# Performance work log

Hardware: AMD Instinct MI355X
Metric: run time of the kernel (lower is better)

## Reference

```python
import jax, jax.numpy as jnp
import numpy as np

B, N, E = 32, 2048, 1048576  # 32 uniform graphs of 2048 nodes, avg degree 16
BN = B * N
KS = (1024, 512, 256)  # TopKPooling ratio=0.5 -> ceil(0.5*n) per layer (uniform graphs -> static)


def _mlp2(x, w1, b1, w2, b2):
    # nn.Sequential(Linear, ReLU, Linear)
    return jnp.maximum(x @ w1 + b1, 0.0) @ w2 + b2


def _forward(x, edge_attr, node_w1, node_b1, node_w2, node_b2,
             edge_w1, edge_b1, edge_w2, edge_b2,
             eff_in_w, eff_in_b, eff_h_w, eff_h_b, eff_out_w, eff_out_b,
             upd_in_w, upd_in_b, upd_h_w, upd_h_b, upd_out_w, upd_out_b,
             pool_w, edge_index):
    relu = lambda t: jnp.maximum(t, 0.0)
    src, dst = edge_index[0], edge_index[1]  # PyG: x_j = h[src], x_i = h[dst], aggregate at dst
    h = _mlp2(x, node_w1, node_b1, node_w2, node_b2)          # [BN, F] node embedding
    e = _mlp2(edge_attr, edge_w1, edge_b1, edge_w2, edge_b2)  # [E, F]  edge embedding
    node_mask = jnp.ones((BN,), bool)
    edge_mask = jnp.ones((E,), bool)
    for i in range(3):
        # --- DPIGNNLayer: gather-concat-MLP(+edge_attr) message, scatter-mean aggregate ---
        m = jnp.concatenate([h[dst], h[src]], axis=-1)        # [E, 2F] = cat(x_i, x_j)
        m = relu(m @ eff_in_w[i] + eff_in_b[i])
        m = relu(m @ eff_h_w[i] + eff_h_b[i])
        m = relu(m @ eff_out_w[i] + eff_out_b[i] + e)
        em = edge_mask.astype(h.dtype)[:, None]
        agg = jax.ops.segment_sum(m * em, dst, num_segments=BN)
        cnt = jax.ops.segment_sum(em, dst, num_segments=BN)
        mean = agg / jnp.maximum(cnt, 1.0)                    # mean aggr (0 where no edges)
        u = jnp.concatenate([mean, h], axis=-1)
        u = relu(u @ upd_in_w[i] + upd_in_b[i])
        u = relu(u @ upd_h_w[i] + upd_h_b[i])
        _ = relu(u @ upd_out_w[i] + upd_out_b[i] + h)  # dead compute: source update() returns x
        # --- TopKPooling(ratio=0.5), masked form (uniform graph sizes -> static k) ---
        w = pool_w[i]
        score = jnp.tanh((h @ w) / jnp.linalg.norm(w))        # [BN]
        masked = jnp.where(node_mask, score, -jnp.inf).reshape(B, N)
        _, idx = jax.lax.top_k(masked, KS[i])                 # [B, k]
        sel = jnp.zeros((B, N), bool).at[jnp.arange(B)[:, None], idx].set(True).reshape(-1)
        node_mask = sel
        h = jnp.where(node_mask[:, None], h * score[:, None], 0.0)
        edge_mask = edge_mask & node_mask[src] & node_mask[dst]  # filter_adj equivalent
    # global_mean_pool over surviving nodes per graph
    nm = node_mask.astype(h.dtype)[:, None]
    sums = (h * nm).reshape(B, N, -1).sum(axis=1)
    cnts = nm.reshape(B, N, 1).sum(axis=1)
    return sums / jnp.maximum(cnts, 1.0)  # [B, F]


def setup_inputs() -> dict:
    key = jax.random.key(0)
    ks = iter(jax.random.split(key, 40))
    F, ND, ED = 128, 16, 8
    s = 0.05
    W = lambda shape: jax.random.normal(next(ks), shape, jnp.float32) * s
    zb = lambda shape: jnp.zeros(shape, jnp.float32)
    e_per = E // B
    base = (jnp.arange(E) // e_per) * N  # graph offset per edge
    src = jax.random.randint(next(ks), (E,), 0, N) + base
    dst = jax.random.randint(next(ks), (E,), 0, N) + base
    return {
        'x': jax.random.normal(next(ks), (BN, ND), jnp.float32),
        'edge_attr': jax.random.normal(next(ks), (E, ED), jnp.float32),
        'node_w1': W((ND, F)), 'node_b1': zb((F,)),
        'node_w2': W((F, F)), 'node_b2': zb((F,)),
        'edge_w1': W((ED, F)), 'edge_b1': zb((F,)),
        'edge_w2': W((F, F)), 'edge_b2': zb((F,)),
        'eff_in_w': W((3, 2 * F, F)), 'eff_in_b': zb((3, F)),
        'eff_h_w': W((3, F, F)), 'eff_h_b': zb((3, F)),
        'eff_out_w': W((3, F, F)), 'eff_out_b': zb((3, F)),
        'upd_in_w': W((3, 2 * F, F)), 'upd_in_b': zb((3, F)),
        'upd_h_w': W((3, F, F)), 'upd_h_b': zb((3, F)),
        'upd_out_w': W((3, F, F)), 'upd_out_b': zb((3, F)),
        'pool_w': W((3, F)),
        'edge_index': jnp.stack([src, dst]),
    }


def reference(x, edge_attr, node_w1, node_b1, node_w2, node_b2,
              edge_w1, edge_b1, edge_w2, edge_b2,
              eff_in_w, eff_in_b, eff_h_w, eff_h_b, eff_out_w, eff_out_b,
              upd_in_w, upd_in_b, upd_h_w, upd_h_b, upd_out_w, upd_out_b,
              pool_w, edge_index):
    return _forward(x, edge_attr, node_w1, node_b1, node_w2, node_b2,
                    edge_w1, edge_b1, edge_w2, edge_b2,
                    eff_in_w, eff_in_b, eff_h_w, eff_h_b, eff_out_w, eff_out_b,
                    upd_in_w, upd_in_b, upd_h_w, upd_h_b, upd_out_w, upd_out_b,
                    pool_w, edge_index)
```

## Files before the change

### kernel.cpp

```cpp
#include <hip/hip_runtime.h>
#include <hip/hip_bf16.h>


#define NPG    2048
#define NGRAPH 32
#define HPAD(b) ((b) + ((b) >> 5))

__global__ __launch_bounds__(256) void k1_fused(
    const float* __restrict__ x,
    const float* __restrict__ W1,
    const float* __restrict__ b1,
    const float* __restrict__ W2,
    const float* __restrict__ b2,
    const float* __restrict__ pw,
    float4* __restrict__ d4)
{
    __shared__ float4 sW1v[512];
    __shared__ float4 sb1v[32];
    __shared__ __align__(16) float swn[384];
    __shared__ __align__(16) float sv[384];
    __shared__ float sc[4];
    __shared__ float snorm[3];
    int t = threadIdx.x;
    int lane = t & 63, wv = t >> 6;

    for (int i = t; i < 512; i += 256) sW1v[i] = ((const float4*)W1)[i];
    if (t < 32) sb1v[t] = ((const float4*)b1)[t];
    if (wv < 3) {
        float w0 = pw[wv * 128 + lane];
        float w1 = pw[wv * 128 + 64 + lane];
        float p = w0 * w0 + w1 * w1;
        #pragma unroll
        for (int s = 32; s; s >>= 1) p += __shfl_xor(p, s);
        if (lane == 0) snorm[wv] = sqrtf(p);
    }
    __syncthreads();
    for (int i = t; i < 384; i += 256) swn[i] = pw[i] / snorm[i >> 7];
    __syncthreads();
    for (int task = t; task < 387; task += 256) {
        int k = task / 129, j = task % 129;
        const float4* r4 = (const float4*)((j < 128) ? (W2 + j * 128) : b2);
        const float* wn = swn + k * 128;
        float p0 = 0.f, p1 = 0.f, p2 = 0.f, p3 = 0.f;
        #pragma unroll 8
        for (int q = 0; q < 32; ++q) {
            float4 w = r4[q];
            p0 = fmaf(w.x, wn[4 * q + 0], p0);
            p1 = fmaf(w.y, wn[4 * q + 1], p1);
            p2 = fmaf(w.z, wn[4 * q + 2], p2);
            p3 = fmaf(w.w, wn[4 * q + 3], p3);
        }
        float p = (p0 + p1) + (p2 + p3);
        if (j < 128) sv[k * 128 + j] = p;
        else sc[k] = p;
    }
    __syncthreads();

    int n = blockIdx.x * 256 + t;
    const float4* xr = (const float4*)(x + (size_t)n * 16);
    float4 xa = xr[0], xb = xr[1], xc = xr[2], xd = xr[3];
    float xs[16] = {xa.x, xa.y, xa.z, xa.w, xb.x, xb.y, xb.z, xb.w,
                    xc.x, xc.y, xc.z, xc.w, xd.x, xd.y, xd.z, xd.w};
    const float4* sv4 = (const float4*)sv;
    float dd0 = sc[0], dd1 = sc[1], dd2 = sc[2];
    #pragma unroll 4
    for (int fq = 0; fq < 32; ++fq) {
        float4 a4 = sb1v[fq];
        #pragma unroll
        for (int j = 0; j < 16; ++j) {
            float4 w = sW1v[j * 32 + fq];
            a4.x = fmaf(xs[j], w.x, a4.x);
            a4.y = fmaf(xs[j], w.y, a4.y);
            a4.z = fmaf(xs[j], w.z, a4.z);
            a4.w = fmaf(xs[j], w.w, a4.w);
        }
        a4.x = fmaxf(a4.x, 0.f); a4.y = fmaxf(a4.y, 0.f);
        a4.z = fmaxf(a4.z, 0.f); a4.w = fmaxf(a4.w, 0.f);
        float4 v0 = sv4[fq], v1 = sv4[32 + fq], v2 = sv4[64 + fq];
        dd0 = fmaf(a4.x, v0.x, fmaf(a4.y, v0.y, fmaf(a4.z, v0.z, fmaf(a4.w, v0.w, dd0))));
        dd1 = fmaf(a4.x, v1.x, fmaf(a4.y, v1.y, fmaf(a4.z, v1.z, fmaf(a4.w, v1.w, dd1))));
        dd2 = fmaf(a4.x, v2.x, fmaf(a4.y, v2.y, fmaf(a4.z, v2.z, fmaf(a4.w, v2.w, dd2))));
    }
    d4[n] = make_float4(dd0, dd1, dd2, 0.f);
}

__global__ __launch_bounds__(1024, 1) void k2_cascade(
    const float* __restrict__ x,
    const float* __restrict__ W1,
    const float* __restrict__ b1,
    const float* __restrict__ W2,
    const float* __restrict__ b2,
    const float4* __restrict__ d4,
    float* __restrict__ out)
{
    __shared__ float d0[NPG], d1[NPG], d2[NPG];
    __shared__ float csc[NPG];
    __shared__ int alive[NPG];
    __shared__ unsigned long long key[NPG];
    __shared__ unsigned int hist[HPAD(2047) + 1];
    __shared__ int sel[256];
    __shared__ float sW1[2048];
    __shared__ float sb1[128];
    __shared__ float Spart[1024];
    __shared__ float Svec[128];
    __shared__ float red4[4];
    __shared__ unsigned long long sPrefix;
    __shared__ int sNeed;
    __shared__ int sCount;
    int t = threadIdx.x;
    int g = blockIdx.x;

    for (int n = t; n < NPG; n += 1024) {
        float4 dd = d4[g * NPG + n];
        d0[n] = dd.x; d1[n] = dd.y; d2[n] = dd.z;
        csc[n] = 1.f; alive[n] = 1;
    }
    for (int i = t; i < 2048; i += 1024) sW1[i] = W1[i];
    if (t < 128) sb1[t] = b1[t];
    if (t == 0) sCount = 0;
    __syncthreads();

    for (int r = 0; r < 3; ++r) {
        int kk = 1024 >> r;
        const float* dr = (r == 0) ? d0 : (r == 1) ? d1 : d2;
        for (int n = t; n < NPG; n += 1024) {
            unsigned long long kv = 0ull;
            if (alive[n]) {
                float z = csc[n] * dr[n];
                unsigned int bb = __float_as_uint(z);
                unsigned int m = (bb & 0x80000000u) ? ~bb : (bb | 0x80000000u);
                kv = ((unsigned long long)m << 11)
                   | (unsigned long long)(unsigned int)(2047 - n);
            }
            key[n] = kv;
        }
        if (t == 0) { sPrefix = 0ull; sNeed = kk; }
        __syncthreads();

        for (int pass = 0; pass < 4; ++pass) {
            int shift = 33 - 11 * pass;
            for (int i = t; i < HPAD(2047) + 1; i += 1024) hist[i] = 0u;
            __syncthreads();
            unsigned long long pref = sPrefix;
            unsigned int need = (unsigned int)sNeed;
            for (int n = t; n < NPG; n += 1024) {
                unsigned long long kv = key[n];
                bool cand = (pass == 0) ||
                            ((kv >> (shift + 11)) == (pref >> (shift + 11)));
                if (cand) {
                    unsigned int dgt = (unsigned int)(kv >> shift) & 2047u;
                    atomicAdd(&hist[HPAD(dgt)], 1u);
                }
            }
            __syncthreads();
            if (t < 64) {
                unsigned int h[32];
                unsigned int tl = 0;
                #pragma unroll
                for (int b = 0; b < 32; ++b) {
                    h[b] = hist[HPAD(32 * t + b)];
                    tl += h[b];
                }
                unsigned int s = tl;
                #pragma unroll
                for (int dlt = 1; dlt < 64; dlt <<= 1) {
                    unsigned int v = __shfl_down(s, dlt);
                    if (t + dlt < 64) s += v;
                }
                unsigned int above = s - tl;
                if (above < need && above + tl >= need) {
                    unsigned int cum = above;
                    #pragma unroll
                    for (int b = 31; b >= 0; --b) {
                        cum += h[b];
                        if (cum >= need) {
                            sNeed = (int)(need - (cum - h[b]));
                            sPrefix = pref |
                                ((unsigned long long)(unsigned int)(32 * t + b) << shift);
                            break;
                        }
                    }
                }
            }
            __syncthreads();
        }
        unsigned long long thr = sPrefix;
        for (int n = t; n < NPG; n += 1024) alive[n] = 0;
        __syncthreads();
        for (int n = t; n < NPG; n += 1024) {
            if (key[n] >= thr) {
                float s = tanhf(csc[n] * dr[n]);
                alive[n] = 1;
                csc[n] *= s;
                if (r == 2) sel[atomicAdd(&sCount, 1)] = n;
            }
        }
        __syncthreads();
    }

    {
        int f = t & 127, half = t >> 7;
        float Sacc = 0.f;
        for (int it = half; it < 256; it += 8) {
            int n = sel[it];
            float cn = csc[n];
            const float4* xr = (const float4*)(x + (size_t)(g * NPG + n) * 16);
            float4 xa = xr[0], xb = xr[1], xc = xr[2], xd = xr[3];
            float acc = sb1[f];
            acc = fmaf(xa.x, sW1[0 * 128 + f], acc);
            acc = fmaf(xa.y, sW1[1 * 128 + f], acc);
            acc = fmaf(xa.z, sW1[2 * 128 + f], acc);
            acc = fmaf(xa.w, sW1[3 * 128 + f], acc);
            acc = fmaf(xb.x, sW1[4 * 128 + f], acc);
            acc = fmaf(xb.y, sW1[5 * 128 + f], acc);
            acc = fmaf(xb.z, sW1[6 * 128 + f], acc);
            acc = fmaf(xb.w, sW1[7 * 128 + f], acc);
            acc = fmaf(xc.x, sW1[8 * 128 + f], acc);
            acc = fmaf(xc.y, sW1[9 * 128 + f], acc);
            acc = fmaf(xc.z, sW1[10 * 128 + f], acc);
            acc = fmaf(xc.w, sW1[11 * 128 + f], acc);
            acc = fmaf(xd.x, sW1[12 * 128 + f], acc);
            acc = fmaf(xd.y, sW1[13 * 128 + f], acc);
            acc = fmaf(xd.z, sW1[14 * 128 + f], acc);
            acc = fmaf(xd.w, sW1[15 * 128 + f], acc);
            Sacc += fmaxf(acc, 0.f) * cn;
        }
        Spart[t] = Sacc;
    }
    if (t < 256) {
        float cpart = csc[sel[t]];
        #pragma unroll
        for (int s = 32; s; s >>= 1) cpart += __shfl_xor(cpart, s);
        if ((t & 63) == 0) red4[t >> 6] = cpart;
    }
    __syncthreads();
    if (t < 128) {
        float sv = 0.f;
        #pragma unroll
        for (int h = 0; h < 8; ++h) sv += Spart[h * 128 + t];
        Svec[t] = sv;
    }
    __syncthreads();
    if (t < 128) {
        float Csum = (red4[0] + red4[1]) + (red4[2] + red4[3]);
        float acc = Csum * b2[t];
        for (int j = 0; j < 128; ++j)
            acc = fmaf(Svec[j], W2[j * 128 + t], acc);
        out[g * 128 + t] = acc * (1.0f / 256.0f);
    }
}

extern "C" void kernel_launch(void* const* d_in, const int* in_sizes, int n_in,
                              void* d_out, int out_size, void* d_ws, size_t ws_size,
                              hipStream_t stream) {
    const float* x  = (const float*)d_in[0];
    const float* W1 = (const float*)d_in[2];
    const float* b1 = (const float*)d_in[3];
    const float* W2 = (const float*)d_in[4];
    const float* b2 = (const float*)d_in[5];
    const float* pw = (const float*)d_in[22];
    float* out = (float*)d_out;

    float4* d4 = (float4*)d_ws;

    k1_fused<<<256, 256, 0, stream>>>(x, W1, b1, W2, b2, pw, d4);
    k2_cascade<<<NGRAPH, 1024, 0, stream>>>(x, W1, b1, W2, b2, d4, out);
}
```

Baseline: 177.6 us.

## Compact survivors between top-k rounds and exit radix select early

After each top-k round, the selected nodes are compacted into dense arrays of index, cumulative score scale and the later-layer dot products, using wave ballot and popcount. The next round then scans only the k survivors instead of all 2048 nodes. The radix select fuses the first histogram into key construction, double-buffers histograms so clearing overlaps the prefix scan, and stops early once the threshold digit is unique. This removes redundant scans and barriers, at the cost of more shared-memory buffers and more complex control flow.

```diff
diff --git a/kernel.cpp b/kernel.cpp
--- a/kernel.cpp
+++ b/kernel.cpp
@@ -4,6 +4,7 @@
 
 #define NPG    2048
 #define NGRAPH 32
+#define HP     2112
 #define HPAD(b) ((b) + ((b) >> 5))
 
 __global__ __launch_bounds__(256) void k1_fused(
@@ -93,79 +94,81 @@
     const float4* __restrict__ d4,
     float* __restrict__ out)
 {
-    __shared__ float d0[NPG], d1[NPG], d2[NPG];
-    __shared__ float csc[NPG];
-    __shared__ int alive[NPG];
-    __shared__ unsigned long long key[NPG];
-    __shared__ unsigned int hist[HPAD(2047) + 1];
-    __shared__ int sel[256];
-    __shared__ float sW1[2048];
-    __shared__ float sb1[128];
-    __shared__ float Spart[1024];
-    __shared__ float Svec[128];
-    __shared__ float red4[4];
+    __shared__ float d0A[NPG], d1A[NPG], d2A[NPG];
+    __shared__ unsigned long long sKey[NPG];
+    __shared__ unsigned int hist[2][HP];
+    __shared__ int   idxB[1024];
+    __shared__ float cscB[1024], d1B[1024], d2B[1024];
+    __shared__ int   idxA2[512];
+    __shared__ float cscA2[512], d2A2[512];
+    __shared__ float sW1[2048], sb1[128];
+    __shared__ float Spart[1024], Svec[128], red4[4];
     __shared__ unsigned long long sPrefix;
-    __shared__ int sNeed;
-    __shared__ int sCount;
-    int t = threadIdx.x;
-    int g = blockIdx.x;
+    __shared__ int sNeed, sDone, sCnt;
+
+    int t = threadIdx.x, g = blockIdx.x;
+    int lane = t & 63, wv = t >> 6;
 
     for (int n = t; n < NPG; n += 1024) {
         float4 dd = d4[g * NPG + n];
-        d0[n] = dd.x; d1[n] = dd.y; d2[n] = dd.z;
-        csc[n] = 1.f; alive[n] = 1;
+        d0A[n] = dd.x; d1A[n] = dd.y; d2A[n] = dd.z;
     }
     for (int i = t; i < 2048; i += 1024) sW1[i] = W1[i];
     if (t < 128) sb1[t] = b1[t];
-    if (t == 0) sCount = 0;
-    __syncthreads();
-
+    for (int i = t; i < 2 * HP; i += 1024) ((unsigned int*)hist)[i] = 0u;
+    __syncthreads();
+
+    int curN = NPG;
     for (int r = 0; r < 3; ++r) {
         int kk = 1024 >> r;
-        const float* dr = (r == 0) ? d0 : (r == 1) ? d1 : d2;
-        for (int n = t; n < NPG; n += 1024) {
-            unsigned long long kv = 0ull;
-            if (alive[n]) {
-                float z = csc[n] * dr[n];
-                unsigned int bb = __float_as_uint(z);
-                unsigned int m = (bb & 0x80000000u) ? ~bb : (bb | 0x80000000u);
-                kv = ((unsigned long long)m << 11)
-                   | (unsigned long long)(unsigned int)(2047 - n);
+        const float* dIn   = (r == 0) ? d0A : (r == 1) ? d1B : d2A2;
+        const float* cscIn = (r == 0) ? (const float*)0 : (r == 1) ? cscB : cscA2;
+        const int*   idxIn = (r == 0) ? (const int*)0 : (r == 1) ? idxB : idxA2;
+        int*   idxOut = (r == 1) ? idxA2 : idxB;
+        float* cscOut = (r == 1) ? cscA2 : cscB;
+
+        if (t == 0) { sPrefix = 0ull; sNeed = kk; sDone = 0; sCnt = 0; }
+        for (int m = t; m < curN; m += 1024) {
+            float ci = cscIn ? cscIn[m] : 1.f;
+            int   ni = idxIn ? idxIn[m] : m;
+            float z = ci * dIn[m];
+            unsigned int bb = __float_as_uint(z);
+            unsigned int mo = (bb & 0x80000000u) ? ~bb : (bb | 0x80000000u);
+            unsigned long long kv = ((unsigned long long)mo << 11)
+                                  | (unsigned long long)(unsigned int)(2047 - ni);
+            sKey[m] = kv;
+            atomicAdd(&hist[0][HPAD((unsigned int)(kv >> 33) & 2047u)], 1u);
+        }
+        __syncthreads();
+
+        int lastBuf = 0;
+        for (int pass = 0; pass < 4; ++pass) {
+            int buf = pass & 1;
+            int shift = 33 - 11 * pass;
+            lastBuf = buf;
+            if (pass > 0) {
+                unsigned long long pref = sPrefix;
+                for (int m = t; m < curN; m += 1024) {
+                    unsigned long long kv = sKey[m];
+                    if ((kv >> (shift + 11)) == (pref >> (shift + 11)))
+                        atomicAdd(&hist[buf][HPAD((unsigned int)(kv >> shift) & 2047u)], 1u);
+                }
+                __syncthreads();
             }
-            key[n] = kv;
-        }
-        if (t == 0) { sPrefix = 0ull; sNeed = kk; }
-        __syncthreads();
-
-        for (int pass = 0; pass < 4; ++pass) {
-            int shift = 33 - 11 * pass;
-            for (int i = t; i < HPAD(2047) + 1; i += 1024) hist[i] = 0u;
-            __syncthreads();
-            unsigned long long pref = sPrefix;
-            unsigned int need = (unsigned int)sNeed;
-            for (int n = t; n < NPG; n += 1024) {
-                unsigned long long kv = key[n];
-                bool cand = (pass == 0) ||
-                            ((kv >> (shift + 11)) == (pref >> (shift + 11)));
-                if (cand) {
-                    unsigned int dgt = (unsigned int)(kv >> shift) & 2047u;
-                    atomicAdd(&hist[HPAD(dgt)], 1u);
-                }
-            }
-            __syncthreads();
-            if (t < 64) {
-                unsigned int h[32];
-                unsigned int tl = 0;
+            if (wv == 0) {
+                unsigned long long pref = sPrefix;
+                unsigned int need = (unsigned int)sNeed;
+                unsigned int h[32], tl = 0;
                 #pragma unroll
                 for (int b = 0; b < 32; ++b) {
-                    h[b] = hist[HPAD(32 * t + b)];
+                    h[b] = hist[buf][HPAD(32u * t + b)];
                     tl += h[b];
                 }
                 unsigned int s = tl;
                 #pragma unroll
-                for (int dlt = 1; dlt < 64; dlt <<= 1) {
-                    unsigned int v = __shfl_down(s, dlt);
-                    if (t + dlt < 64) s += v;
+                for (int d = 1; d < 64; d <<= 1) {
+                    unsigned int v = __shfl_down(s, d);
+                    if (t + d < 64) s += v;
                 }
                 unsigned int above = s - tl;
                 if (above < need && above + tl >= need) {
@@ -174,36 +177,57 @@
                     for (int b = 31; b >= 0; --b) {
                         cum += h[b];
                         if (cum >= need) {
-                            sNeed = (int)(need - (cum - h[b]));
+                            int nn = (int)(need - (cum - h[b]));
+                            sNeed = nn;
                             sPrefix = pref |
                                 ((unsigned long long)(unsigned int)(32 * t + b) << shift);
+                            sDone = (nn == (int)h[b]) || (pass == 3);
                             break;
                         }
                     }
                 }
+            } else if (pass > 0) {
+                for (int i = t - 64; i < HP; i += 960) hist[buf ^ 1][i] = 0u;
             }
             __syncthreads();
+            if (sDone) break;
         }
         unsigned long long thr = sPrefix;
-        for (int n = t; n < NPG; n += 1024) alive[n] = 0;
+
+        for (int i = t; i < HP; i += 1024) hist[lastBuf][i] = 0u;
+        for (int m = t; m < curN; m += 1024) {
+            unsigned long long kv = sKey[m];
+            bool pred = (kv >= thr);
+            unsigned long long mask = __ballot(pred);
+            if (mask) {
+                int leader = __ffsll((long long)mask) - 1;
+                int cnt = __popcll(mask);
+                int base = 0;
+                if (lane == leader) base = atomicAdd(&sCnt, cnt);
+                base = __shfl(base, leader);
+                if (pred) {
+                    int rank = __popcll(mask & ((1ull << lane) - 1ull));
+                    int pos = base + rank;
+                    float ci = cscIn ? cscIn[m] : 1.f;
+                    int   ni = idxIn ? idxIn[m] : m;
+                    float z = ci * dIn[m];
+                    idxOut[pos] = ni;
+                    cscOut[pos] = ci * tanhf(z);
+                    if (r == 0)      { d1B[pos] = d1A[m]; d2B[pos] = d2A[m]; }
+                    else if (r == 1) { d2A2[pos] = d2B[m]; }
+                }
+            }
+        }
         __syncthreads();
-        for (int n = t; n < NPG; n += 1024) {
-            if (key[n] >= thr) {
-                float s = tanhf(csc[n] * dr[n]);
-                alive[n] = 1;
-                csc[n] *= s;
-                if (r == 2) sel[atomicAdd(&sCount, 1)] = n;
-            }
-        }
-        __syncthreads();
+        curN = kk;
     }
 
     {
-        int f = t & 127, half = t >> 7;
+        int f = t & 127, grp = t >> 7;
         float Sacc = 0.f;
-        for (int it = half; it < 256; it += 8) {
-            int n = sel[it];
-            float cn = csc[n];
+        for (int it = grp; it < 256; it += 8) {
+            int n = idxB[it];
+            float cn = cscB[it];
             const float4* xr = (const float4*)(x + (size_t)(g * NPG + n) * 16);
             float4 xa = xr[0], xb = xr[1], xc = xr[2], xd = xr[3];
             float acc = sb1[f];
@@ -228,7 +252,7 @@
         Spart[t] = Sacc;
     }
     if (t < 256) {
-        float cpart = csc[sel[t]];
+        float cpart = cscB[t];
         #pragma unroll
         for (int s = 32; s; s >>= 1) cpart += __shfl_xor(cpart, s);
         if ((t & 63) == 0) red4[t >> 6] = cpart;
```

Result: faster. 168.2 us (-5.3%).
